# Performance work log

Measured on AMD Instinct MI355X. Metric: run time of the kernel, lower is better.

Reference implementation:

```python
import jax, jax.numpy as jnp
import numpy as np

B, FEAT, HID, LAT, NQ, NEMB = 2048, 840, 256, 128, 12, 512


def setup_inputs() -> dict:
    key = jax.random.key(0)
    ks = jax.random.split(key, 6)
    return {
        "x": jax.random.normal(ks[0], (B, FEAT), jnp.float32),
        "w1": jax.random.normal(ks[1], (HID, 1, 3), jnp.float32) * 0.1,   # Conv1d(1->256, k=3)
        "b1": jnp.zeros((HID,), jnp.float32),
        "w2": jax.random.normal(ks[2], (LAT, HID, 3), jnp.float32) * 0.05,  # Conv1d(256->128, k=3)
        "b2": jnp.zeros((LAT,), jnp.float32),
        # 12 codebooks of (512, 128), init uniform(-1/n_emb, 1/n_emb) per the torch code
        "codebooks": jax.random.uniform(ks[3], (NQ, NEMB, LAT), jnp.float32, -1.0 / NEMB, 1.0 / NEMB),
    }


def _encode(x, w1, b1, w2, b2):
    # x: (B, FEAT) -> unsqueeze channel dim -> NCW conv stack -> adaptive avg pool(1)
    h = x[:, None, :]  # (B, 1, FEAT)
    h = jax.lax.conv_general_dilated(h, w1, (1,), 'SAME',
                                     dimension_numbers=('NCH', 'OIH', 'NCH'))
    h = jax.nn.relu(h + b1[None, :, None])
    h = jax.lax.conv_general_dilated(h, w2, (1,), 'SAME',
                                     dimension_numbers=('NCH', 'OIH', 'NCH'))
    h = jax.nn.relu(h + b2[None, :, None])
    return h.mean(axis=2)  # AdaptiveAvgPool1d(1) + squeeze -> (B, LAT)


def _rvq(z_flat, codebooks):
    # sequential residual VQ: 12 stages of cdist -> argmin -> gather -> residual update
    def step(residual, cb):
        # squared L2 distances: ||r||^2 - 2 r C^T + ||c||^2, shape (B, NEMB)
        d = (jnp.sum(residual ** 2, axis=1, keepdims=True)
             - 2.0 * (residual @ cb.T)
             + jnp.sum(cb ** 2, axis=1)[None, :])
        idx = jnp.argmin(d, axis=1)          # (B,)
        q = cb[idx]                          # (B, LAT) embedding gather
        residual = residual - jax.lax.stop_gradient(q)  # .detach() in torch
        return residual, (q, idx)

    _, (qs, idxs) = jax.lax.scan(step, z_flat, codebooks)  # qs: (NQ, B, LAT)
    return qs.sum(axis=0), idxs.T  # (B, LAT), (B, NQ)


def reference(x, w1, b1, w2, b2, codebooks):
    z = _encode(x, w1, b1, w2, b2)            # (B, LAT)
    zq, idx = _rvq(z, codebooks)              # L = 1 so flat == (B, LAT)
    return zq[:, None, :], idx[:, None, :]    # (B, 1, LAT), (B, 1, NQ)
```

## Files before the change

kernel.cpp:

```cpp
#include <hip/hip_runtime.h>

#define B_SZ 2048
#define FEAT 840
#define HID  256
#define LAT  128
#define NQ   12
#define NEMB 512

#define T_SUB 40
#define NTILE 21
#define HSTR  46
#define H2STR 41
#define CHALF 128
#define HBUF  (CHALF * HSTR)

#define W2R_FLOATS ((size_t)HID * 384)
#define CBN_FLOATS ((size_t)NQ * NEMB)

__device__ __forceinline__ float np8_combine(const float* r) {
    float sA = __fadd_rn(r[0], r[1]);
    float sB = __fadd_rn(r[2], r[3]);
    float sC = __fadd_rn(r[4], r[5]);
    float sD = __fadd_rn(r[6], r[7]);
    return __fadd_rn(__fadd_rn(sA, sB), __fadd_rn(sC, sD));
}

__global__ __launch_bounds__(256) void w2r_kernel(const float* __restrict__ w2,
                                                  float* __restrict__ w2r)
{
    int p = blockIdx.x * 256 + threadIdx.x;
    if (p >= HID * 384) return;
    int c2 = p / 384, r = p - c2 * 384;
    int ly = r / 12, jk = r - ly * 12;
    int j = jk / 3, k = jk - j * 3;
    w2r[p] = w2[(size_t)(ly*4 + j)*768 + c2*3 + k];
}

__global__ __launch_bounds__(256) void cbn_kernel(const float* __restrict__ cb,
                                                  float* __restrict__ cbn)
{
    int p = blockIdx.x * 256 + threadIdx.x;
    if (p >= NQ * NEMB) return;
    const float* __restrict__ cp = cb + (size_t)p * LAT;
    float c8[8];
#pragma unroll
    for (int j = 0; j < 8; ++j) {
        float c = cp[j];
        c8[j] = __fmul_rn(c, c);
    }
    for (int i = 8; i < LAT; i += 8)
#pragma unroll
        for (int j = 0; j < 8; ++j) {
            float c = cp[i+j];
            c8[j] = __fadd_rn(c8[j], __fmul_rn(c, c));
        }
    cbn[p] = np8_combine(c8);
}

template <int USE_WR>
__global__ __launch_bounds__(256) void enc_kernel(
    const float* __restrict__ x,  const float* __restrict__ w1,
    const float* __restrict__ b1, const float* __restrict__ w2,
    const float* __restrict__ w2r,
    const float* __restrict__ b2, float* __restrict__ zout)
{
    __shared__ float xp[2][FEAT + 4];
    __shared__ float h1s[2][HBUF];
    __shared__ float leafs[2][LAT * 8];

    const int tid  = threadIdx.x;
    const int half = tid >> 7;
    const int htid = tid & 127;
    const int b    = blockIdx.x * 2 + half;

    const int tx  = htid & 3;
    const int ly  = htid >> 2;
    const int u0  = tx * 10;

    const int ach = htid;

    float* __restrict__ xph = xp[half];
    float* __restrict__ h1h = h1s[half];
    float* __restrict__ lfh = leafs[half];

    float b2v[4];
#pragma unroll
    for (int j = 0; j < 4; ++j) b2v[j] = b2[ly*4 + j];

    for (int i = htid; i < FEAT + 2; i += 128)
        xph[i] = (i >= 1 && i <= FEAT) ? x[(size_t)b*FEAT + i - 1] : 0.f;

    float racc[8];
    int leaf_id = 0, leaf_pos = 0;
#pragma unroll
    for (int j = 0; j < 8; ++j) racc[j] = 0.f;

    __syncthreads();
    for (int t0 = 0; t0 < FEAT; t0 += T_SUB) {
        const bool edge = (t0 == 0) | (t0 + T_SUB == FEAT);

        float sk[4][10][3];
#pragma unroll
        for (int j = 0; j < 4; ++j)
#pragma unroll
            for (int i = 0; i < 10; ++i)
#pragma unroll
                for (int k = 0; k < 3; ++k) sk[j][i][k] = 0.f;

#pragma unroll 1
        for (int hf = 0; hf < 2; ++hf) {
            {
                const int c = hf*CHALF + ach;
                const float wA = w1[c*3+0], wB = w1[c*3+1], wC = w1[c*3+2];
                const float bb = b1[c];
                if (edge) {
                    for (int tp = 0; tp < T_SUB + 2; ++tp) {
                        int tg = t0 - 1 + tp;
                        float v = 0.f;
                        if (tg >= 0 && tg < FEAT) {
                            float s = __fadd_rn(__fadd_rn(__fmul_rn(wA, xph[tg]),
                                                          __fmul_rn(wB, xph[tg+1])),
                                                __fmul_rn(wC, xph[tg+2]));
                            s = __fadd_rn(s, bb);
                            v = s > 0.f ? s : 0.f;
                        }
                        h1h[ach*HSTR + tp] = v;
                    }
                } else {
#pragma unroll 6
                    for (int tp = 0; tp < T_SUB + 2; ++tp) {
                        int tg = t0 - 1 + tp;
                        float s = __fadd_rn(__fadd_rn(__fmul_rn(wA, xph[tg]),
                                                      __fmul_rn(wB, xph[tg+1])),
                                            __fmul_rn(wC, xph[tg+2]));
                        s = __fadd_rn(s, bb);
                        h1h[ach*HSTR + tp] = s > 0.f ? s : 0.f;
                    }
                }
            }
            __syncthreads();

            if (USE_WR) {
                const float* __restrict__ wbase =
                    w2r + (size_t)(hf*CHALF)*384 + ly*12;
#pragma unroll 2
                for (int cc = 0; cc < CHALF; ++cc) {
                    const float4* __restrict__ wq =
                        (const float4*)(wbase + (size_t)cc*384);
                    float4 A0 = wq[0], A1 = wq[1], A2 = wq[2];
                    float w_[12];
                    w_[0]=A0.x; w_[1]=A0.y; w_[2]=A0.z; w_[3]=A0.w;
                    w_[4]=A1.x; w_[5]=A1.y; w_[6]=A1.z; w_[7]=A1.w;
                    w_[8]=A2.x; w_[9]=A2.y; w_[10]=A2.z; w_[11]=A2.w;

                    const float2* __restrict__ hq =
                        (const float2*)(&h1h[cc*HSTR + u0]);
                    float2 q0=hq[0], q1=hq[1], q2=hq[2], q3=hq[3], q4=hq[4], q5=hq[5];
                    float hv[12] = {q0.x,q0.y,q1.x,q1.y,q2.x,q2.y,
                                    q3.x,q3.y,q4.x,q4.y,q5.x,q5.y};
#pragma unroll
                    for (int j = 0; j < 4; ++j)
#pragma unroll
                        for (int i = 0; i < 10; ++i)
#pragma unroll
                            for (int k = 0; k < 3; ++k)
                                sk[j][i][k] = __fmaf_rn(w_[j*3+k], hv[i+k],
                                                        sk[j][i][k]);
                }
            } else {
                for (int cc = 0; cc < CHALF; ++cc) {
                    int c2 = hf*CHALF + cc;
                    const float* hp = &h1h[cc*HSTR + u0];
                    float hv[12];
#pragma unroll
                    for (int m = 0; m < 12; ++m) hv[m] = hp[m];
#pragma unroll
                    for (int j = 0; j < 4; ++j) {
                        float wa = w2[(size_t)(ly*4+j)*768 + c2*3 + 0];
                        float wb = w2[(size_t)(ly*4+j)*768 + c2*3 + 1];
                        float wc = w2[(size_t)(ly*4+j)*768 + c2*3 + 2];
#pragma unroll
                        for (int i = 0; i < 10; ++i) {
                            sk[j][i][0] = __fmaf_rn(wa, hv[i],   sk[j][i][0]);
                            sk[j][i][1] = __fmaf_rn(wb, hv[i+1], sk[j][i][1]);
                            sk[j][i][2] = __fmaf_rn(wc, hv[i+2], sk[j][i][2]);
                        }
                    }
                }
            }
            __syncthreads();
        }

#pragma unroll
        for (int j = 0; j < 4; ++j)
#pragma unroll
            for (int i = 0; i < 10; ++i) {
                float hh = __fadd_rn(__fadd_rn(sk[j][i][0], sk[j][i][1]),
                                     sk[j][i][2]);
                hh = __fadd_rn(hh, b2v[j]);
                hh = hh > 0.f ? hh : 0.f;
                h1h[(ly*4 + j)*H2STR + u0 + i] = hh;
            }
        __syncthreads();

        for (int g = 0; g < T_SUB; g += 8) {
            float v[8];
#pragma unroll
            for (int m = 0; m < 8; ++m)
                v[m] = h1h[htid*H2STR + g + m];
#pragma unroll
            for (int m = 0; m < 8; ++m) {
                float vv = v[m];
                int j = leaf_pos & 7;
                racc[j] = (leaf_pos < 8) ? vv : __fadd_rn(racc[j], vv);
                ++leaf_pos;
                int llen = (leaf_id == 7) ? 112 : 104;
                if (leaf_pos == llen) {
                    lfh[htid*8 + leaf_id] = np8_combine(racc);
                    ++leaf_id; leaf_pos = 0;
                }
            }
        }
        __syncthreads();
    }

    {
        const float* L = &lfh[htid*8];
        float s0 = __fadd_rn(L[0], L[1]);
        float s1 = __fadd_rn(L[2], L[3]);
        float sA = __fadd_rn(s0, s1);
        float s2 = __fadd_rn(L[4], L[5]);
        float s3 = __fadd_rn(L[6], L[7]);
        float sB = __fadd_rn(s2, s3);
        float tot = __fadd_rn(sA, sB);
        zout[(size_t)b*LAT + htid] = __fdiv_rn(tot, 840.0f);
    }
}

template <int USE_CN>
__global__ __launch_bounds__(256) void rvq32_kernel(
    const float* __restrict__ cb, const float* __restrict__ cbn,
    const float* __restrict__ z,
    float* __restrict__ zqout, float* __restrict__ oidx)
{
    __shared__ float rr[LAT];
    __shared__ float Ash;
    __shared__ float redd[256];
    __shared__ int   rede[256];
    __shared__ float sredd[64];
    __shared__ int   srede[64];
    __shared__ int   beste;
    __shared__ float qv[NQ * LAT];

    const int tid = threadIdx.x;
    const int b   = blockIdx.x;

    if (tid < LAT) rr[tid] = z[(size_t)b*LAT + tid];
    __syncthreads();

    for (int q = 0; q < NQ; ++q) {
        const float* __restrict__ cbq = cb + (size_t)q * NEMB * LAT;

        if (tid == 0) {
            float r8[8];
#pragma unroll
            for (int j = 0; j < 8; ++j) r8[j] = __fmul_rn(rr[j], rr[j]);
            for (int i = 8; i < LAT; i += 8)
#pragma unroll
                for (int j = 0; j < 8; ++j)
                    r8[j] = __fadd_rn(r8[j], __fmul_rn(rr[i+j], rr[i+j]));
            Ash = np8_combine(r8);
        }
        __syncthreads();

        float dmin = 0.f; int emin = 0;
#pragma unroll
        for (int h = 0; h < 2; ++h) {
            int e = 2*tid + h;
            const float* __restrict__ cp = cbq + (size_t)e*LAT;
            float dot = 0.f;
            float cn;
            if (USE_CN) {
#pragma unroll
                for (int j = 0; j < 8; ++j)
                    dot = __fmaf_rn(cp[j], rr[j], dot);
                for (int i = 8; i < LAT; i += 8)
#pragma unroll
                    for (int j = 0; j < 8; ++j)
                        dot = __fmaf_rn(cp[i+j], rr[i+j], dot);
                cn = cbn[(size_t)q*NEMB + e];
            } else {
                float c8[8];
#pragma unroll
                for (int j = 0; j < 8; ++j) {
                    float c = cp[j];
                    c8[j] = __fmul_rn(c, c);
                    dot = __fmaf_rn(c, rr[j], dot);
                }
                for (int i = 8; i < LAT; i += 8)
#pragma unroll
                    for (int j = 0; j < 8; ++j) {
                        float c = cp[i+j];
                        dot = __fmaf_rn(c, rr[i+j], dot);
                        c8[j] = __fadd_rn(c8[j], __fmul_rn(c, c));
                    }
                cn = np8_combine(c8);
            }
            float G  = __fmul_rn(2.0f, dot);
            float d  = __fadd_rn(__fsub_rn(Ash, G), cn);
            if (h == 0) { dmin = d; emin = e; }
            else if (d < dmin) { dmin = d; emin = e; }
        }
        redd[tid] = dmin; rede[tid] = emin;
        __syncthreads();

        if (tid < 64) {
            float bb = redd[tid*4]; int ee = rede[tid*4];
            for (int j = 1; j < 4; ++j) {
                float dj = redd[tid*4 + j];
                if (dj < bb) { bb = dj; ee = rede[tid*4 + j]; }
            }
            sredd[tid] = bb; srede[tid] = ee;
        }
        __syncthreads();
        if (tid == 0) {
            float bb = sredd[0]; int ee = srede[0];
            for (int j = 1; j < 64; ++j) {
                float dj = sredd[j];
                if (dj < bb) { bb = dj; ee = srede[j]; }
            }
            beste = ee;
            oidx[(size_t)b*NQ + q] = (float)ee;
        }
        __syncthreads();

        if (tid < LAT) {
            float cv = cbq[(size_t)beste*LAT + tid];
            qv[q*LAT + tid] = cv;
            rr[tid] = __fsub_rn(rr[tid], cv);
        }
        __syncthreads();
    }

    if (tid < LAT) {
        float s = qv[tid];
        for (int s2 = 1; s2 < NQ; ++s2)
            s = __fadd_rn(s, qv[s2*LAT + tid]);
        zqout[(size_t)b*LAT + tid] = s;
    }
}

extern "C" void kernel_launch(void* const* d_in, const int* in_sizes, int n_in,
                              void* d_out, int out_size, void* d_ws, size_t ws_size,
                              hipStream_t stream)
{
    (void)in_sizes; (void)n_in; (void)out_size;
    const float* x  = (const float*)d_in[0];
    const float* w1 = (const float*)d_in[1];
    const float* b1 = (const float*)d_in[2];
    const float* w2 = (const float*)d_in[3];
    const float* b2 = (const float*)d_in[4];
    const float* cb = (const float*)d_in[5];

    float* out  = (float*)d_out;
    float* zq   = out;
    float* oidx = out + (size_t)B_SZ * LAT;

    const size_t w2r_bytes  = W2R_FLOATS * sizeof(float);
    const size_t full_bytes = (W2R_FLOATS + CBN_FLOATS) * sizeof(float);

    if (ws_size >= full_bytes) {
        float* w2r = (float*)d_ws;
        float* cbn = (float*)d_ws + W2R_FLOATS;
        w2r_kernel<<<(HID*384 + 255)/256, 256, 0, stream>>>(w2, w2r);
        cbn_kernel<<<(NQ*NEMB + 255)/256, 256, 0, stream>>>(cb, cbn);
        enc_kernel<1><<<B_SZ/2, 256, 0, stream>>>(x, w1, b1, w2, w2r, b2, zq);
        rvq32_kernel<1><<<B_SZ, 256, 0, stream>>>(cb, cbn, zq, zq, oidx);
    } else if (ws_size >= w2r_bytes) {
        float* w2r = (float*)d_ws;
        w2r_kernel<<<(HID*384 + 255)/256, 256, 0, stream>>>(w2, w2r);
        enc_kernel<1><<<B_SZ/2, 256, 0, stream>>>(x, w1, b1, w2, w2r, b2, zq);
        rvq32_kernel<0><<<B_SZ, 256, 0, stream>>>(cb, nullptr, zq, zq, oidx);
    } else {
        enc_kernel<0><<<B_SZ/2, 256, 0, stream>>>(x, w1, b1, w2, nullptr, b2, zq);
        rvq32_kernel<0><<<B_SZ, 256, 0, stream>>>(cb, nullptr, zq, zq, oidx);
    }
}
```

Baseline: 5.136 ms.

## Double encoder threads per sample and transpose w2 layout for coalesced loads

The encoder block grows from 256 to 512 threads. Each thread now computes 2 output channels instead of 4 for conv2, and conv1 rows are split between two threads. The reordered w2 layout places consecutive lanes' weights contiguously, so the per-channel weight loads are coalesced scalar loads instead of per-thread float4 strided loads. This halves register accumulators per thread, which should raise occupancy and parallelism. In exchange, half the threads sit idle during the pooling phase, and each h1 value in shared memory is read by twice as many lanes per channel.

```diff
diff --git a/kernel.cpp b/kernel.cpp
--- a/kernel.cpp
+++ b/kernel.cpp
@@ -14,7 +14,7 @@
 #define CHALF 128
 #define HBUF  (CHALF * HSTR)
 
-#define W2R_FLOATS ((size_t)HID * 384)
+#define W2T_FLOATS ((size_t)HID * 384)
 #define CBN_FLOATS ((size_t)NQ * NEMB)
 
 __device__ __forceinline__ float np8_combine(const float* r) {
@@ -26,14 +26,14 @@
 }
 
 __global__ __launch_bounds__(256) void w2r_kernel(const float* __restrict__ w2,
-                                                  float* __restrict__ w2r)
+                                                  float* __restrict__ w2t)
 {
     int p = blockIdx.x * 256 + threadIdx.x;
     if (p >= HID * 384) return;
     int c2 = p / 384, r = p - c2 * 384;
-    int ly = r / 12, jk = r - ly * 12;
-    int j = jk / 3, k = jk - j * 3;
-    w2r[p] = w2[(size_t)(ly*4 + j)*768 + c2*3 + k];
+    int m = r / 64, ly = r - m * 64;
+    int j = m / 3, k = m - j * 3;
+    w2t[p] = w2[(size_t)(2*ly + j)*768 + c2*3 + k];
 }
 
 __global__ __launch_bounds__(256) void cbn_kernel(const float* __restrict__ cb,
@@ -58,10 +58,10 @@
 }
 
 template <int USE_WR>
-__global__ __launch_bounds__(256) void enc_kernel(
+__global__ __launch_bounds__(512) void enc_kernel(
     const float* __restrict__ x,  const float* __restrict__ w1,
     const float* __restrict__ b1, const float* __restrict__ w2,
-    const float* __restrict__ w2r,
+    const float* __restrict__ w2t,
     const float* __restrict__ b2, float* __restrict__ zout)
 {
     __shared__ float xp[2][FEAT + 4];
@@ -69,25 +69,26 @@
     __shared__ float leafs[2][LAT * 8];
 
     const int tid  = threadIdx.x;
-    const int half = tid >> 7;
-    const int htid = tid & 127;
+    const int half = tid >> 8;
+    const int htid = tid & 255;
     const int b    = blockIdx.x * 2 + half;
 
-    const int tx  = htid & 3;
-    const int ly  = htid >> 2;
-    const int u0  = tx * 10;
-
-    const int ach = htid;
+    const int ly = htid & 63;
+    const int tx = htid >> 6;
+    const int u0 = tx * 10;
+
+    const int ach   = htid >> 1;
+    const int piece = htid & 1;
 
     float* __restrict__ xph = xp[half];
     float* __restrict__ h1h = h1s[half];
     float* __restrict__ lfh = leafs[half];
 
-    float b2v[4];
-#pragma unroll
-    for (int j = 0; j < 4; ++j) b2v[j] = b2[ly*4 + j];
-
-    for (int i = htid; i < FEAT + 2; i += 128)
+    float b2v[2];
+    b2v[0] = b2[2*ly + 0];
+    b2v[1] = b2[2*ly + 1];
+
+    for (int i = htid; i < FEAT + 2; i += 256)
         xph[i] = (i >= 1 && i <= FEAT) ? x[(size_t)b*FEAT + i - 1] : 0.f;
 
     float racc[8];
@@ -99,9 +100,9 @@
     for (int t0 = 0; t0 < FEAT; t0 += T_SUB) {
         const bool edge = (t0 == 0) | (t0 + T_SUB == FEAT);
 
-        float sk[4][10][3];
-#pragma unroll
-        for (int j = 0; j < 4; ++j)
+        float sk[2][10][3];
+#pragma unroll
+        for (int j = 0; j < 2; ++j)
 #pragma unroll
             for (int i = 0; i < 10; ++i)
 #pragma unroll
@@ -113,8 +114,9 @@
                 const int c = hf*CHALF + ach;
                 const float wA = w1[c*3+0], wB = w1[c*3+1], wC = w1[c*3+2];
                 const float bb = b1[c];
+                const int tpb = piece * 21;
                 if (edge) {
-                    for (int tp = 0; tp < T_SUB + 2; ++tp) {
+                    for (int tp = tpb; tp < tpb + 21; ++tp) {
                         int tg = t0 - 1 + tp;
                         float v = 0.f;
                         if (tg >= 0 && tg < FEAT) {
@@ -127,8 +129,8 @@
                         h1h[ach*HSTR + tp] = v;
                     }
                 } else {
-#pragma unroll 6
-                    for (int tp = 0; tp < T_SUB + 2; ++tp) {
+#pragma unroll 7
+                    for (int tp = tpb; tp < tpb + 21; ++tp) {
                         int tg = t0 - 1 + tp;
                         float s = __fadd_rn(__fadd_rn(__fmul_rn(wA, xph[tg]),
                                                       __fmul_rn(wB, xph[tg+1])),
@@ -141,25 +143,25 @@
             __syncthreads();
 
             if (USE_WR) {
-                const float* __restrict__ wbase =
-                    w2r + (size_t)(hf*CHALF)*384 + ly*12;
+                const float* __restrict__ wp =
+                    w2t + (size_t)(hf*CHALF)*384 + ly;
 #pragma unroll 2
                 for (int cc = 0; cc < CHALF; ++cc) {
-                    const float4* __restrict__ wq =
-                        (const float4*)(wbase + (size_t)cc*384);
-                    float4 A0 = wq[0], A1 = wq[1], A2 = wq[2];
-                    float w_[12];
-                    w_[0]=A0.x; w_[1]=A0.y; w_[2]=A0.z; w_[3]=A0.w;
-                    w_[4]=A1.x; w_[5]=A1.y; w_[6]=A1.z; w_[7]=A1.w;
-                    w_[8]=A2.x; w_[9]=A2.y; w_[10]=A2.z; w_[11]=A2.w;
+                    const float* __restrict__ wv = wp + (size_t)cc*384;
+                    float w_[6];
+#pragma unroll
+                    for (int m = 0; m < 6; ++m) w_[m] = wv[m*64];
 
                     const float2* __restrict__ hq =
                         (const float2*)(&h1h[cc*HSTR + u0]);
-                    float2 q0=hq[0], q1=hq[1], q2=hq[2], q3=hq[3], q4=hq[4], q5=hq[5];
-                    float hv[12] = {q0.x,q0.y,q1.x,q1.y,q2.x,q2.y,
-                                    q3.x,q3.y,q4.x,q4.y,q5.x,q5.y};
-#pragma unroll
-                    for (int j = 0; j < 4; ++j)
+                    float hv[12];
+#pragma unroll
+                    for (int m = 0; m < 6; ++m) {
+                        float2 q = hq[m];
+                        hv[2*m] = q.x; hv[2*m+1] = q.y;
+                    }
+#pragma unroll
+                    for (int j = 0; j < 2; ++j)
 #pragma unroll
                         for (int i = 0; i < 10; ++i)
 #pragma unroll
@@ -175,10 +177,10 @@
 #pragma unroll
                     for (int m = 0; m < 12; ++m) hv[m] = hp[m];
 #pragma unroll
-                    for (int j = 0; j < 4; ++j) {
-                        float wa = w2[(size_t)(ly*4+j)*768 + c2*3 + 0];
-                        float wb = w2[(size_t)(ly*4+j)*768 + c2*3 + 1];
-                        float wc = w2[(size_t)(ly*4+j)*768 + c2*3 + 2];
+                    for (int j = 0; j < 2; ++j) {
+                        float wa = w2[(size_t)(2*ly+j)*768 + c2*3 + 0];
+                        float wb = w2[(size_t)(2*ly+j)*768 + c2*3 + 1];
+                        float wc = w2[(size_t)(2*ly+j)*768 + c2*3 + 2];
 #pragma unroll
                         for (int i = 0; i < 10; ++i) {
                             sk[j][i][0] = __fmaf_rn(wa, hv[i],   sk[j][i][0]);
@@ -192,39 +194,41 @@
         }
 
 #pragma unroll
-        for (int j = 0; j < 4; ++j)
+        for (int j = 0; j < 2; ++j)
 #pragma unroll
             for (int i = 0; i < 10; ++i) {
                 float hh = __fadd_rn(__fadd_rn(sk[j][i][0], sk[j][i][1]),
                                      sk[j][i][2]);
                 hh = __fadd_rn(hh, b2v[j]);
                 hh = hh > 0.f ? hh : 0.f;
-                h1h[(ly*4 + j)*H2STR + u0 + i] = hh;
-            }
-        __syncthreads();
-
-        for (int g = 0; g < T_SUB; g += 8) {
-            float v[8];
-#pragma unroll
-            for (int m = 0; m < 8; ++m)
-                v[m] = h1h[htid*H2STR + g + m];
-#pragma unroll
-            for (int m = 0; m < 8; ++m) {
-                float vv = v[m];
-                int j = leaf_pos & 7;
-                racc[j] = (leaf_pos < 8) ? vv : __fadd_rn(racc[j], vv);
-                ++leaf_pos;
-                int llen = (leaf_id == 7) ? 112 : 104;
-                if (leaf_pos == llen) {
-                    lfh[htid*8 + leaf_id] = np8_combine(racc);
-                    ++leaf_id; leaf_pos = 0;
-                }
-            }
-        }
-        __syncthreads();
-    }
-
-    {
+                h1h[(2*ly + j)*H2STR + u0 + i] = hh;
+            }
+        __syncthreads();
+
+        if (htid < LAT) {
+            for (int g = 0; g < T_SUB; g += 8) {
+                float v[8];
+#pragma unroll
+                for (int m = 0; m < 8; ++m)
+                    v[m] = h1h[htid*H2STR + g + m];
+#pragma unroll
+                for (int m = 0; m < 8; ++m) {
+                    float vv = v[m];
+                    int j = leaf_pos & 7;
+                    racc[j] = (leaf_pos < 8) ? vv : __fadd_rn(racc[j], vv);
+                    ++leaf_pos;
+                    int llen = (leaf_id == 7) ? 112 : 104;
+                    if (leaf_pos == llen) {
+                        lfh[htid*8 + leaf_id] = np8_combine(racc);
+                        ++leaf_id; leaf_pos = 0;
+                    }
+                }
+            }
+        }
+        __syncthreads();
+    }
+
+    if (htid < LAT) {
         const float* L = &lfh[htid*8];
         float s0 = __fadd_rn(L[0], L[1]);
         float s1 = __fadd_rn(L[2], L[3]);
@@ -366,23 +370,23 @@
     float* zq   = out;
     float* oidx = out + (size_t)B_SZ * LAT;
 
-    const size_t w2r_bytes  = W2R_FLOATS * sizeof(float);
-    const size_t full_bytes = (W2R_FLOATS + CBN_FLOATS) * sizeof(float);
+    const size_t w2t_bytes  = W2T_FLOATS * sizeof(float);
+    const size_t full_bytes = (W2T_FLOATS + CBN_FLOATS) * sizeof(float);
 
     if (ws_size >= full_bytes) {
-        float* w2r = (float*)d_ws;
-        float* cbn = (float*)d_ws + W2R_FLOATS;
-        w2r_kernel<<<(HID*384 + 255)/256, 256, 0, stream>>>(w2, w2r);
+        float* w2t = (float*)d_ws;
+        float* cbn = (float*)d_ws + W2T_FLOATS;
+        w2r_kernel<<<(HID*384 + 255)/256, 256, 0, stream>>>(w2, w2t);
         cbn_kernel<<<(NQ*NEMB + 255)/256, 256, 0, stream>>>(cb, cbn);
-        enc_kernel<1><<<B_SZ/2, 256, 0, stream>>>(x, w1, b1, w2, w2r, b2, zq);
+        enc_kernel<1><<<B_SZ/2, 512, 0, stream>>>(x, w1, b1, w2, w2t, b2, zq);
         rvq32_kernel<1><<<B_SZ, 256, 0, stream>>>(cb, cbn, zq, zq, oidx);
-    } else if (ws_size >= w2r_bytes) {
-        float* w2r = (float*)d_ws;
-        w2r_kernel<<<(HID*384 + 255)/256, 256, 0, stream>>>(w2, w2r);
-        enc_kernel<1><<<B_SZ/2, 256, 0, stream>>>(x, w1, b1, w2, w2r, b2, zq);
+    } else if (ws_size >= w2t_bytes) {
+        float* w2t = (float*)d_ws;
+        w2r_kernel<<<(HID*384 + 255)/256, 256, 0, stream>>>(w2, w2t);
+        enc_kernel<1><<<B_SZ/2, 512, 0, stream>>>(x, w1, b1, w2, w2t, b2, zq);
         rvq32_kernel<0><<<B_SZ, 256, 0, stream>>>(cb, nullptr, zq, zq, oidx);
     } else {
-        enc_kernel<0><<<B_SZ/2, 256, 0, stream>>>(x, w1, b1, w2, nullptr, b2, zq);
+        enc_kernel<0><<<B_SZ/2, 512, 0, stream>>>(x, w1, b1, w2, nullptr, b2, zq);
         rvq32_kernel<0><<<B_SZ, 256, 0, stream>>>(cb, nullptr, zq, zq, oidx);
     }
 }
```

After: 5.966 ms. 1.16x slower.
